# Performance work log

Hardware: AMD Instinct MI355X
Metric: run time of the kernel (lower is better)

## Reference

```python
import jax, jax.numpy as jnp
import numpy as np

B = 64
D_IN = 4000            # reduced from hardcoded 40000 to fit memory budget (see notes)
N_NODES = 200
ADJ = N_NODES * N_NODES  # 40000 entries per adjacency
E_PER = ADJ // 4         # strictly > 0.75-quantile of 40000 continuous values == top 10000
NEG_SLOPE = 0.2          # GATv2Conv default leaky_relu slope
LN_EPS = 1e-5


def _gelu(x):
    return jax.nn.gelu(x, approximate=False)  # torch F.gelu default = exact erf


def _gatv2(x, src, dst, valid, Wl, bl, Wr, br, att, bias, heads, ch, concat, n):
    # PyG GATv2Conv (share_weights=False): xl = lin_l(x), xr = lin_r(x)
    xl = (x @ Wl + bl).reshape(n, heads, ch)
    xr = (x @ Wr + br).reshape(n, heads, ch)
    e = jax.nn.leaky_relu(xl[src] + xr[dst], NEG_SLOPE)        # [E,H,C]
    logits = jnp.einsum('ehc,hc->eh', e, att)                   # [E,H]
    if valid is not None:
        logits = jnp.where(valid[:, None], logits, -jnp.inf)
    m = jax.ops.segment_max(logits, dst, num_segments=n)
    m = jnp.where(jnp.isfinite(m), m, 0.0)
    ex = jnp.exp(logits - m[dst])
    if valid is not None:
        ex = jnp.where(valid[:, None], ex, 0.0)
    denom = jax.ops.segment_sum(ex, dst, num_segments=n)
    alpha = ex / (denom[dst] + 1e-16)                            # scatter-softmax per target
    out = jax.ops.segment_sum(xl[src] * alpha[..., None], dst, num_segments=n)
    out = out.reshape(n, heads * ch) if concat else out.mean(axis=1)
    return out + bias


def _forward(raw_fc, gbW, gbb, feW1, feb1, feW2, feb2, ln_g, ln_b,
             W1l, b1l, W1r, b1r, att1, bias1,
             W2l, b2l, W2r, b2r, att2, bias2,
             W3l, b3l, W3r, b3r, att3, bias3):
    b = raw_fc.shape[0]
    n = b * N_NODES
    # ---- build_graph ----
    adj = jax.nn.sigmoid(raw_fc @ gbW + gbb).reshape(b, N_NODES, N_NODES)
    adj = (adj + jnp.swapaxes(adj, 1, 2)) * 0.5
    means = adj.mean(axis=2)                    # [B,200]
    stds = jnp.std(adj, axis=2, ddof=1) + 1e-6  # torch std is unbiased
    base = jnp.stack([means, stds], axis=-1).reshape(n, 2)
    h = _gelu(base @ feW1 + feb1) @ feW2 + feb2
    mu = h.mean(-1, keepdims=True)
    var = h.var(-1, keepdims=True)
    x = (h - mu) / jnp.sqrt(var + LN_EPS) * ln_g + ln_b          # LayerNorm(16)
    _, idx = jax.lax.top_k(adj.reshape(b, ADJ), E_PER)           # [B, 10000]
    row = idx // N_NODES
    col = idx % N_NODES
    offs = (jnp.arange(b) * N_NODES)[:, None]
    src = (row + offs).reshape(-1)
    dst = (col + offs).reshape(-1)
    # ---- GAT stack (eval mode: dropout = identity) ----
    x = _gelu(_gatv2(x, src, dst, None, W1l, b1l, W1r, b1r, att1, bias1, 8, 128, True, n))
    # layers 2/3 have add_self_loops=True: remove existing self loops, append one per node
    loops = jnp.arange(n)
    src2 = jnp.concatenate([src, loops])
    dst2 = jnp.concatenate([dst, loops])
    valid2 = jnp.concatenate([src != dst, jnp.ones((n,), bool)])
    x = _gelu(_gatv2(x, src2, dst2, valid2, W2l, b2l, W2r, b2r, att2, bias2, 4, 256, True, n))
    x = _gelu(_gatv2(x, src2, dst2, valid2, W3l, b3l, W3r, b3r, att3, bias3, 1, 512, False, n))
    # global_mean_pool: exactly 200 nodes per graph, contiguous ordering
    return x.reshape(b, N_NODES, 512).mean(axis=1)


def setup_inputs() -> dict:
    key = jax.random.key(0)
    ks = jax.random.split(key, 16)
    f32 = jnp.float32
    def gl(k, shape, fan_in):
        return jax.random.normal(k, shape, f32) / np.sqrt(fan_in)
    inp = {}
    inp['raw_fc'] = jax.random.normal(ks[0], (B, D_IN), f32)
    inp['gbW'] = gl(ks[1], (D_IN, ADJ), D_IN)
    inp['gbb'] = jnp.zeros((ADJ,), f32)
    inp['feW1'] = gl(ks[2], (2, 8), 2);      inp['feb1'] = jnp.zeros((8,), f32)
    inp['feW2'] = gl(ks[3], (8, 16), 8);     inp['feb2'] = jnp.zeros((16,), f32)
    inp['ln_g'] = jnp.ones((16,), f32);      inp['ln_b'] = jnp.zeros((16,), f32)
    inp['W1l'] = gl(ks[4], (16, 8 * 128), 16);   inp['b1l'] = jnp.zeros((8 * 128,), f32)
    inp['W1r'] = gl(ks[5], (16, 8 * 128), 16);   inp['b1r'] = jnp.zeros((8 * 128,), f32)
    inp['att1'] = gl(ks[6], (8, 128), 128);      inp['bias1'] = jnp.zeros((8 * 128,), f32)
    inp['W2l'] = gl(ks[7], (1024, 4 * 256), 1024); inp['b2l'] = jnp.zeros((4 * 256,), f32)
    inp['W2r'] = gl(ks[8], (1024, 4 * 256), 1024); inp['b2r'] = jnp.zeros((4 * 256,), f32)
    inp['att2'] = gl(ks[9], (4, 256), 256);        inp['bias2'] = jnp.zeros((4 * 256,), f32)
    inp['W3l'] = gl(ks[10], (1024, 512), 1024);    inp['b3l'] = jnp.zeros((512,), f32)
    inp['W3r'] = gl(ks[11], (1024, 512), 1024);    inp['b3r'] = jnp.zeros((512,), f32)
    inp['att3'] = gl(ks[12], (1, 512), 512);       inp['bias3'] = jnp.zeros((512,), f32)
    return inp


def reference(raw_fc, gbW, gbb, feW1, feb1, feW2, feb2, ln_g, ln_b,
              W1l, b1l, W1r, b1r, att1, bias1,
              W2l, b2l, W2r, b2r, att2, bias2,
              W3l, b3l, W3r, b3r, att3, bias3):
    return _forward(raw_fc, gbW, gbb, feW1, feb1, feW2, feb2, ln_g, ln_b,
                    W1l, b1l, W1r, b1r, att1, bias1,
                    W2l, b2l, W2r, b2r, att2, bias2,
                    W3l, b3l, W3r, b3r, att3, bias3)
```

## Files before the change

### kernel.cpp

```cpp
#include <hip/hip_runtime.h>
#include <hip/hip_fp16.h>
#include <math.h>
#include <cstdint>
#include <cstddef>

#define NGRAPH 64
#define NN 200
#define ADJN 40000
#define DIN 4000
#define NNODE 12800

typedef float    f32x4 __attribute__((ext_vector_type(4)));
typedef _Float16 f16x8 __attribute__((ext_vector_type(8)));
typedef _Float16 f16x4 __attribute__((ext_vector_type(4)));
typedef _Float16 f16x2 __attribute__((ext_vector_type(2)));
typedef short    bf8v  __attribute__((ext_vector_type(8)));
typedef short    bf4v  __attribute__((ext_vector_type(4)));

union BF8U  { bf8v v; bf4v h[2]; };
union F16X8U{ f16x8 v; f16x4 h[2]; f16x2 p[4]; };
union U4F   { uint4 u; unsigned w[4]; };

__device__ __forceinline__ unsigned short f2bf(float f) {
  unsigned u = __float_as_uint(f);
  return (unsigned short)((u + 0x7fffu + ((u >> 16) & 1u)) >> 16);
}
__device__ __forceinline__ float bf2f(unsigned short s) {
  return __uint_as_float(((unsigned)s) << 16);
}
__device__ __forceinline__ float gelu_f(float x) {
  return x * 0.5f * (1.0f + erff(x * 0.70710678118654752f));
}

#if defined(__has_builtin)
#if __has_builtin(__builtin_amdgcn_fdot2)
#define FDOT2(a, b, c) __builtin_amdgcn_fdot2((a), (b), (c), false)
#endif
#endif
#ifndef FDOT2
#define FDOT2(a, b, c) ((c) + (float)(a)[0] * (float)(b)[0] + (float)(a)[1] * (float)(b)[1])
#endif

__device__ __forceinline__ void glds16(const _Float16* g, _Float16* l) {
  __builtin_amdgcn_global_load_lds(
      (const __attribute__((address_space(1))) void*)g,
      (__attribute__((address_space(3))) void*)l, 16, 0, 0);
}

__global__ __launch_bounds__(256) void prep_A(const float* __restrict__ A,
                                              short* __restrict__ Ahi,
                                              short* __restrict__ Alo) {
  const int i = blockIdx.x * 256 + threadIdx.x;
  const float v = A[i];
  const unsigned short h = f2bf(v);
  Ahi[i] = (short)h;
  Alo[i] = (short)f2bf(v - bf2f(h));
}

__global__ __launch_bounds__(256) void transp_all(
    const float* __restrict__ W2l, const float* __restrict__ W2r,
    const float* __restrict__ W3l, const float* __restrict__ W3r,
    _Float16* __restrict__ T2l, _Float16* __restrict__ T2r,
    _Float16* __restrict__ T3l, _Float16* __restrict__ T3r) {
  __shared__ float tile[32][33];
  const int z = blockIdx.z;
  if (z >= 2 && blockIdx.y >= 16) return;
  const float* src = (z == 0) ? W2l : (z == 1) ? W2r : (z == 2) ? W3l : W3r;
  _Float16* dst = (z == 0) ? T2l : (z == 1) ? T2r : (z == 2) ? T3l : T3r;
  const int N = (z < 2) ? 1024 : 512;
  const int K = 1024;
  const int bk = blockIdx.x * 32, bn = blockIdx.y * 32;
  const int tx = threadIdx.x & 31, ty = threadIdx.x >> 5;
#pragma unroll
  for (int r = 0; r < 32; r += 8) tile[ty + r][tx] = src[(size_t)(bk + ty + r) * N + bn + tx];
  __syncthreads();
#pragma unroll
  for (int r = 0; r < 32; r += 8)
    dst[(size_t)(bn + ty + r) * K + bk + tx] = (_Float16)tile[tx][ty + r];
}

#define BA_LOADW(WV, K0)                                                        \
  _Pragma("unroll") for (int q = 0; q < 8; ++q)                                 \
    WV[q] = W[(size_t)((K0) + kgrp * 8 + q) * ADJN + n0 + nn];

#define BA_CONV(PB, WV)                                                         \
  { bf4v h0, h1, l0, l1;                                                        \
    _Pragma("unroll") for (int i = 0; i < 4; ++i) {                             \
      unsigned short hh = (unsigned short)(__float_as_uint(WV[i]) >> 16);       \
      h0[i] = (short)hh;                                                        \
      l0[i] = (short)f2bf(WV[i] - bf2f(hh));                                    \
    }                                                                           \
    _Pragma("unroll") for (int i = 0; i < 4; ++i) {                             \
      unsigned short hh = (unsigned short)(__float_as_uint(WV[4 + i]) >> 16);   \
      h1[i] = (short)hh;                                                        \
      l1[i] = (short)f2bf(WV[4 + i] - bf2f(hh));                                \
    }                                                                           \
    *(bf4v*)(Wh[PB] + nn * 44 + kgrp * 8)     = h0;                             \
    *(bf4v*)(Wh[PB] + nn * 44 + kgrp * 8 + 4) = h1;                             \
    *(bf4v*)(Wl[PB] + nn * 44 + kgrp * 8)     = l0;                             \
    *(bf4v*)(Wl[PB] + nn * 44 + kgrp * 8 + 4) = l1;                             \
  }

#define BA_MFMA(PB, AHC, ALC)                                                   \
  _Pragma("unroll") for (int j = 0; j < 4; ++j) {                               \
    const int bc = (j * 16 + (lane & 15)) * 44 + kb;                            \
    BF8U bh, bl;                                                                \
    bh.h[0] = *(const bf4v*)(Wh[PB] + bc);                                      \
    bh.h[1] = *(const bf4v*)(Wh[PB] + bc + 4);                                  \
    bl.h[0] = *(const bf4v*)(Wl[PB] + bc);                                      \
    bl.h[1] = *(const bf4v*)(Wl[PB] + bc + 4);                                  \
    acc[j] = __builtin_amdgcn_mfma_f32_16x16x32_bf16(AHC, bh.v, acc[j], 0, 0, 0); \
    acc[j] = __builtin_amdgcn_mfma_f32_16x16x32_bf16(AHC, bl.v, acc[j], 0, 0, 0); \
    acc[j] = __builtin_amdgcn_mfma_f32_16x16x32_bf16(ALC, bh.v, acc[j], 0, 0, 0); \
  }

#define BA_LOADA(AH, AL, K0)                                                    \
  AH = *(const bf8v*)(Ahi + (size_t)arow * DIN + (K0) + kb);                    \
  AL = *(const bf8v*)(Alo + (size_t)arow * DIN + (K0) + kb);

__global__ __launch_bounds__(256) void build_adj(
    const short* __restrict__ Ahi, const short* __restrict__ Alo,
    const float* __restrict__ W, const float* __restrict__ bias,
    float* __restrict__ adj) {
  __shared__ short Wh[2][64 * 44], Wl[2][64 * 44];
  const int t = threadIdx.x, wave = t >> 6, lane = t & 63;
  const int n0 = blockIdx.x * 64;
  const int nn = t & 63, kgrp = t >> 6;
  const int kb = (lane >> 4) * 8;
  const int arow = wave * 16 + (lane & 15);
  f32x4 acc[4] = {};
  float wva[8], wvb[8];
  bf8v ahs0, als0, ahs1, als1;
  BA_LOADW(wva, 0)
  BA_LOADA(ahs0, als0, 0)
  BA_LOADW(wvb, 32)
  BA_LOADA(ahs1, als1, 32)
  BA_CONV(0, wva)
  for (int it = 0; it < 124; it += 2) {
    __syncthreads();
    {
      const bf8v ahc = ahs0, alc = als0;
      if (it + 2 < 125) {
        const int k2 = (it + 2) * 32;
        BA_LOADW(wva, k2)
        BA_LOADA(ahs0, als0, k2)
      }
      BA_MFMA(0, ahc, alc)
      BA_CONV(1, wvb)
    }
    __syncthreads();
    {
      const bf8v ahc = ahs1, alc = als1;
      if (it + 3 < 125) {
        const int k2 = (it + 3) * 32;
        BA_LOADW(wvb, k2)
        BA_LOADA(ahs1, als1, k2)
      }
      BA_MFMA(1, ahc, alc)
      if (it + 2 < 125) BA_CONV(0, wva)
    }
  }
  __syncthreads();
  BA_MFMA(0, ahs0, als0)
#pragma unroll
  for (int j = 0; j < 4; ++j) {
    const int col = n0 + j * 16 + (lane & 15);
    const float bb = bias[col];
#pragma unroll
    for (int vv = 0; vv < 4; ++vv) {
      const int row = wave * 16 + (lane >> 4) * 4 + vv;
      float x = acc[j][vv] + bb;
      adj[(size_t)row * ADJN + col] = 1.0f / (1.0f + __expf(-x));
    }
  }
}

__global__ __launch_bounds__(256) void symmetrize(const float* __restrict__ adj,
                                                  float* __restrict__ adjS) {
  __shared__ float tl[64][65];
  const int g = blockIdx.x;
  const int i0 = (blockIdx.y >> 2) * 64, j0 = (blockIdx.y & 3) * 64;
  const int tx = threadIdx.x & 63, ty = threadIdx.x >> 6;
  const float* ag = adj + (size_t)g * ADJN;
#pragma unroll
  for (int r = 0; r < 64; r += 4) {
    const int jr = j0 + ty + r;
    tl[ty + r][tx] = (jr < NN && i0 + tx < NN) ? ag[jr * NN + i0 + tx] : 0.f;
  }
  __syncthreads();
#pragma unroll
  for (int r = 0; r < 64; r += 4) {
    const int i = i0 + ty + r, j = j0 + tx;
    if (i < NN && j < NN)
      adjS[(size_t)g * ADJN + i * NN + j] = 0.5f * (ag[i * NN + j] + tl[tx][ty + r]);
  }
}

__global__ __launch_bounds__(256) void rowstats(const float* __restrict__ adjS,
                                                float* __restrict__ meanv,
                                                float* __restrict__ stdv) {
  const int row = blockIdx.x * 4 + (threadIdx.x >> 6);
  const int lane = threadIdx.x & 63;
  const float* r = adjS + (size_t)row * NN;
  float s = 0.f, q = 0.f;
#pragma unroll
  for (int k = 0; k < 4; ++k) {
    int i = k * 64 + lane;
    if (i < NN) { float v = r[i]; s += v; q += v * v; }
  }
#pragma unroll
  for (int off = 32; off > 0; off >>= 1) { s += __shfl_xor(s, off); q += __shfl_xor(q, off); }
  if (lane == 0) {
    float m = s * (1.0f / 200.0f);
    float var = (q - 200.0f * m * m) * (1.0f / 199.0f);
    var = fmaxf(var, 0.f);
    meanv[row] = m;
    stdv[row] = sqrtf(var) + 1e-6f;
  }
}

__global__ __launch_bounds__(1024) void radix_lists(
    const float* __restrict__ adjS,
    int* __restrict__ cnt1, int* __restrict__ cnt2,
    unsigned char* __restrict__ list1, unsigned char* __restrict__ list2) {
  __shared__ unsigned hist[4 * 2048];
  __shared__ unsigned s_pref, s_cA;
  const int g = blockIdx.x, t = threadIdx.x, lane = t & 63, wave = t >> 6;
  const float* v = adjS + (size_t)g * ADJN;
  unsigned prefix = 0, pmask = 0, cA = 0;
  const int shifts[3] = {20, 9, 0};
  const int widths[3] = {2048, 2048, 512};
  for (int pass = 0; pass < 3; ++pass) {
    const int nb = widths[pass], sh = shifts[pass];
    for (int i = t; i < 8192; i += 1024) hist[i] = 0u;
    __syncthreads();
    const int cpy = (lane & 3) * 2048;
    for (int e = t; e < ADJN; e += 1024) {
      unsigned u = __float_as_uint(v[e]);
      if ((u & pmask) == prefix) atomicAdd(&hist[cpy + ((u >> sh) & (nb - 1))], 1u);
    }
    __syncthreads();
    if (t < 64) {
      const int CH = nb >> 6;
      unsigned lsum = 0;
      for (int i = 0; i < CH; ++i) {
        const int b = t * CH + i;
        lsum += hist[b] + hist[2048 + b] + hist[4096 + b] + hist[6144 + b];
      }
      unsigned s = lsum;
#pragma unroll
      for (int off = 1; off < 64; off <<= 1) {
        unsigned o = __shfl_down(s, off);
        if (lane + off < 64) s += o;
      }
      const unsigned need = 10000u - cA;
      unsigned sn = __shfl_down(s, 1);
      const unsigned snext = (lane == 63) ? 0u : sn;
      if (s >= need && snext < need) {
        unsigned cum = snext;
        int bsel = t * CH;
        for (int i = CH - 1; i >= 0; --i) {
          const int b = t * CH + i;
          unsigned hb = hist[b] + hist[2048 + b] + hist[4096 + b] + hist[6144 + b];
          if (cum + hb >= need) { bsel = b; break; }
          cum += hb;
        }
        s_pref = prefix | ((unsigned)bsel << sh);
        s_cA = cA + cum;
      }
    }
    __syncthreads();
    prefix = s_pref; cA = s_cA;
    pmask |= (unsigned)(widths[pass] - 1) << sh;
    __syncthreads();
  }
  const float tv = __uint_as_float(prefix);
  for (int j = wave; j < NN; j += 16) {
    const float* row = adjS + (size_t)g * ADJN + (size_t)j * NN;
    unsigned char* l1 = list1 + ((size_t)g * NN + j) * NN;
    unsigned char* l2 = list2 + ((size_t)g * NN + j) * NN;
    int c1 = 0, c2 = 0;
#pragma unroll
    for (int r = 0; r < 4; ++r) {
      int i = r * 64 + lane;
      bool p1 = false, p2 = false;
      if (i < NN) { float vv = row[i]; p1 = (vv >= tv); p2 = p1 && (i != j); }
      unsigned long long b1 = __ballot(p1);
      unsigned long long b2 = __ballot(p2);
      unsigned long long below = (lane == 0) ? 0ull : ((~0ull) >> (64 - lane));
      if (p1) l1[c1 + __popcll(b1 & below)] = (unsigned char)i;
      if (p2) l2[c2 + __popcll(b2 & below)] = (unsigned char)i;
      c1 += (int)__popcll(b1); c2 += (int)__popcll(b2);
    }
    if (lane == 0) {
      l2[c2] = (unsigned char)j;
      cnt1[g * NN + j] = c1;
      cnt2[g * NN + j] = c2 + 1;
    }
  }
}

__global__ __launch_bounds__(256) void lin16_fused(
    const float* __restrict__ meanv, const float* __restrict__ stdv,
    const float* __restrict__ feW1, const float* __restrict__ feb1,
    const float* __restrict__ feW2, const float* __restrict__ feb2,
    const float* __restrict__ ln_g, const float* __restrict__ ln_b,
    const float* __restrict__ Wl, const float* __restrict__ bl,
    const float* __restrict__ Wr, const float* __restrict__ br,
    _Float16* __restrict__ outl, _Float16* __restrict__ outr) {
  __shared__ _Float16 Wt[1024 * 20];
  __shared__ float x0s[16][17];
  const int t = threadIdx.x, wave = t >> 6, lane = t & 63;
  const int mbase = blockIdx.x * 16;
  {
    const int n = t >> 4, o = t & 15;
    const float mu = meanv[mbase + n], sd = stdv[mbase + n];
    float h1[8];
#pragma unroll
    for (int k = 0; k < 8; ++k) h1[k] = gelu_f(mu * feW1[k] + sd * feW1[8 + k] + feb1[k]);
    float h2 = feb2[o];
#pragma unroll
    for (int k = 0; k < 8; ++k) h2 += h1[k] * feW2[k * 16 + o];
    float s = h2;
#pragma unroll
    for (int off = 1; off < 16; off <<= 1) s += __shfl_xor(s, off);
    s *= (1.0f / 16.0f);
    const float d = h2 - s;
    float vv = d * d;
#pragma unroll
    for (int off = 1; off < 16; off <<= 1) vv += __shfl_xor(vv, off);
    vv *= (1.0f / 16.0f);
    x0s[n][o] = d * (1.0f / sqrtf(vv + 1e-5f)) * ln_g[o] + ln_b[o];
  }
  __syncthreads();
  const int mrow = lane & 15, kg = lane >> 4;
  F16X8U af;
#pragma unroll
  for (int q = 0; q < 8; ++q) af.v[q] = (_Float16)0.f;
  if (kg < 2) {
#pragma unroll
    for (int q = 0; q < 8; ++q) af.v[q] = (_Float16)x0s[mrow][kg * 8 + q];
  }
#pragma unroll
  for (int mat = 0; mat < 2; ++mat) {
    if (mat) __syncthreads();
    const float* Wsrc = mat ? Wr : Wl;
    for (int i = t; i < 4096; i += 256) {
      const int k = i >> 8, n4 = (i & 255) * 4;
      float4 wv = *(const float4*)(Wsrc + (size_t)k * 1024 + n4);
      Wt[(n4 + 0) * 20 + k] = (_Float16)wv.x;
      Wt[(n4 + 1) * 20 + k] = (_Float16)wv.y;
      Wt[(n4 + 2) * 20 + k] = (_Float16)wv.z;
      Wt[(n4 + 3) * 20 + k] = (_Float16)wv.w;
    }
    __syncthreads();
    const float* bias = mat ? br : bl;
    _Float16* out = mat ? outr : outl;
#pragma unroll
    for (int nt = 0; nt < 16; ++nt) {
      const int n0 = wave * 256 + nt * 16;
      F16X8U bfv;
#pragma unroll
      for (int q = 0; q < 8; ++q) bfv.v[q] = (_Float16)0.f;
      if (kg < 2) bfv.v = *(const f16x8*)(Wt + (n0 + mrow) * 20 + kg * 8);
      f32x4 acc = {};
      acc = __builtin_amdgcn_mfma_f32_16x16x32_f16(af.v, bfv.v, acc, 0, 0, 0);
      const int col = n0 + mrow;
      const float bb = bias[col];
#pragma unroll
      for (int j = 0; j < 4; ++j)
        out[(size_t)(mbase + kg * 4 + j) * 1024 + col] = (_Float16)(acc[j] + bb);
    }
  }
}

__global__ __launch_bounds__(256, 2) void gemm_nt(
    const _Float16* __restrict__ A,
    const _Float16* __restrict__ Bt0, const _Float16* __restrict__ Bt1,
    const float* __restrict__ b0, const float* __restrict__ b1,
    _Float16* __restrict__ out0, _Float16* __restrict__ out1,
    int Nhalf, int tilesPerHalf) {
  __shared__ _Float16 As[2][128 * 64];
  __shared__ _Float16 Bs[2][128 * 64];
  const int mbase = blockIdx.y * 128;
  const int hsel = blockIdx.x / tilesPerHalf;
  const int ncol0 = (blockIdx.x % tilesPerHalf) * 128;
  const _Float16* Bt = hsel ? Bt1 : Bt0;
  const float* bias = hsel ? b1 : b0;
  _Float16* out = hsel ? out1 : out0;
  const int t = threadIdx.x, wave = t >> 6, lane = t & 63;
  const int wm = wave >> 1, wn = wave & 1;
  f32x4 acc[4][4] = {};
  const int srow = lane >> 3;
  const int sg = (lane & 7) ^ srow;
#pragma unroll
  for (int c = 0; c < 4; ++c) {
    const int rbase = wave * 32 + c * 8;
    glds16(A + (size_t)(mbase + rbase + srow) * 1024 + sg * 8, As[0] + rbase * 64);
    glds16(Bt + (size_t)(ncol0 + rbase + srow) * 1024 + sg * 8, Bs[0] + rbase * 64);
  }
  __syncthreads();
  for (int kt = 0; kt < 16; ++kt) {
    const int p = kt & 1;
    if (kt < 15) {
      const int k0 = (kt + 1) * 64;
#pragma unroll
      for (int c = 0; c < 4; ++c) {
        const int rbase = wave * 32 + c * 8;
        glds16(A + (size_t)(mbase + rbase + srow) * 1024 + k0 + sg * 8, As[p ^ 1] + rbase * 64);
        glds16(Bt + (size_t)(ncol0 + rbase + srow) * 1024 + k0 + sg * 8, Bs[p ^ 1] + rbase * 64);
      }
    }
#pragma unroll
    for (int ks = 0; ks < 2; ++ks) {
      F16X8U af[4], bfv[4];
#pragma unroll
      for (int m = 0; m < 4; ++m) {
        const int row = wm * 64 + m * 16 + (lane & 15);
        const int kk = ks * 32 + (lane >> 4) * 8;
        af[m].v = *(const f16x8*)(As[p] + row * 64 + (kk ^ ((row & 7) << 3)));
      }
#pragma unroll
      for (int j = 0; j < 4; ++j) {
        const int row = wn * 64 + j * 16 + (lane & 15);
        const int kk = ks * 32 + (lane >> 4) * 8;
        bfv[j].v = *(const f16x8*)(Bs[p] + row * 64 + (kk ^ ((row & 7) << 3)));
      }
#pragma unroll
      for (int j = 0; j < 4; ++j)
#pragma unroll
        for (int m = 0; m < 4; ++m)
          acc[m][j] = __builtin_amdgcn_mfma_f32_16x16x32_f16(af[m].v, bfv[j].v, acc[m][j], 0, 0, 0);
    }
    __syncthreads();
  }
#pragma unroll
  for (int j = 0; j < 4; ++j) {
    const int col = ncol0 + wn * 64 + j * 16 + (lane & 15);
    const float bb = bias[col];
#pragma unroll
    for (int m = 0; m < 4; ++m) {
#pragma unroll
      for (int vv = 0; vv < 4; ++vv) {
        const int row = mbase + wm * 64 + m * 16 + (lane >> 4) * 4 + vv;
        out[(size_t)row * Nhalf + col] = (_Float16)(acc[m][j][vv] + bb);
      }
    }
  }
}

template <int C, int HC>
__global__ __launch_bounds__(1024, 4) void gat_layer(
    const _Float16* __restrict__ xlb, const _Float16* __restrict__ xrb,
    const float* __restrict__ attw, const float* __restrict__ biasw,
    const int* __restrict__ cnts, const unsigned char* __restrict__ lists,
    _Float16* __restrict__ outb) {
  extern __shared__ char smem[];
  constexpr int XLB = 200 * C * 2;
  constexpr int XRW = 16 * C * 2;
  _Float16* xr_s = (_Float16*)(smem + XLB);
  unsigned* awp = (unsigned*)(smem + XLB + XRW);
  unsigned* att_s = (unsigned*)(smem + XLB + XRW + 12800);
  const int g = blockIdx.x;
  const int hd = blockIdx.y;
  const int t = threadIdx.x, wave = t >> 6, lane = t & 63;
  constexpr int NGR = C / 8;
  constexpr int GRP = (C == 128) ? 16 : 32;
  constexpr int NG = 64 / GRP;
  const int grp = lane / GRP, li = lane % GRP;
  const int rc = lane & (NGR - 1) & 31;

  for (int ch = t; ch < 200 * NGR; ch += 1024) {
    const int node = ch / NGR, cc = (ch % NGR) * 8;
    *(f16x8*)(smem + (node * C + cc) * 2) =
        *(const f16x8*)(xlb + (size_t)(g * 200 + node) * HC + hd * C + cc);
  }
  for (int i = t; i < C / 2; i += 1024) {
    f16x2 a;
    a[0] = (_Float16)attw[hd * C + 2 * i];
    a[1] = (_Float16)attw[hd * C + 2 * i + 1];
    att_s[i] = __builtin_bit_cast(unsigned, a);
  }
  __syncthreads();

  _Float16* xr_w = xr_s + wave * C;
  const uint4* att4 = (const uint4*)att_s;
  f16x8 xrreg;
  if (lane < NGR)
    xrreg = *(const f16x8*)(xrb + (size_t)(g * 200 + wave) * HC + hd * C + lane * 8);

  for (int jj = wave; jj < 200; jj += 16) {
    const int gn = g * 200 + jj;
    const int cnt = cnts[gn];
    const unsigned char* lst = lists + (size_t)gn * NN;
    if (lane < NGR) {
      *(f16x8*)(xr_w + lane * 8) = xrreg;
      if (jj + 16 < 200)
        xrreg = *(const f16x8*)(xrb + (size_t)(gn + 16) * HC + hd * C + lane * 8);
    }
    float lg[4] = {-INFINITY, -INFINITY, -INFINITY, -INFINITY};
    int sreg[4];
#pragma unroll
    for (int r = 0; r < 4; ++r) {
      const int e = (r << 6) + lane;
      if (e < cnt) {
        const int s = lst[e];
        sreg[r] = s;
        const _Float16* xrow = (const _Float16*)(smem) + s * C;
        float accv[4] = {0.f, 0.f, 0.f, 0.f};
#pragma unroll 4
        for (int gi0 = 0; gi0 < NGR; ++gi0) {
          const int gi = (gi0 + rc) & (NGR - 1);
          const int cc = gi * 8;
          F16X8U xa, raa;
          xa.v = *(const f16x8*)(xrow + cc);
          raa.v = *(const f16x8*)(xr_w + cc);
          U4F av; av.u = att4[gi];
#pragma unroll
          for (int pq = 0; pq < 4; ++pq) {
            f16x2 z = xa.p[pq] + raa.p[pq];
            f16x2 zs = z * (_Float16)0.2f;
            f16x2 m = __builtin_elementwise_max(z, zs);
            accv[pq] = FDOT2(__builtin_bit_cast(f16x2, av.w[pq]), m, accv[pq]);
          }
        }
        lg[r] = (accv[0] + accv[1]) + (accv[2] + accv[3]);
      }
    }
    float mloc = fmaxf(fmaxf(lg[0], lg[1]), fmaxf(lg[2], lg[3]));
#pragma unroll
    for (int off = 32; off > 0; off >>= 1) mloc = fmaxf(mloc, __shfl_xor(mloc, off));
    float ex[4]; float ps = 0.f;
#pragma unroll
    for (int r = 0; r < 4; ++r) { ex[r] = __expf(lg[r] - mloc); ps += ex[r]; }
#pragma unroll
    for (int off = 32; off > 0; off >>= 1) ps += __shfl_xor(ps, off);
    const float denom = ps + 1e-16f;
#pragma unroll
    for (int r = 0; r < 4; ++r) {
      const int e = (r << 6) + lane;
      if (e < cnt) {
        const unsigned short ab =
            __builtin_bit_cast(unsigned short, (_Float16)(ex[r] / denom));
        awp[wave * 200 + e] = ((unsigned)ab << 16) | (unsigned)sreg[r];
      }
    }
    float o[8] = {};
    for (int e0 = 0; e0 < cnt; e0 += NG) {
      const int e = e0 + grp;
      if (e < cnt) {
        const unsigned v = awp[wave * 200 + e];
        const int s = v & 0xFF;
        const float a =
            (float)__builtin_bit_cast(_Float16, (unsigned short)(v >> 16));
        f16x8 xv = *(const f16x8*)((const _Float16*)smem + s * C + li * 8);
#pragma unroll
        for (int q = 0; q < 8; ++q) o[q] += a * (float)xv[q];
      }
    }
#pragma unroll
    for (int q = 0; q < 8; ++q) {
      if constexpr (GRP == 16) o[q] += __shfl_xor(o[q], 16);
      o[q] += __shfl_xor(o[q], 32);
    }
    if (grp == 0) {
      const int colb = hd * C + li * 8;
      f16x8 ov;
#pragma unroll
      for (int q = 0; q < 8; ++q) ov[q] = (_Float16)gelu_f(o[q] + biasw[colb + q]);
      *(f16x8*)(outb + (size_t)gn * HC + colb) = ov;
    }
  }
}

__global__ __launch_bounds__(1024, 4) void gat_l3(
    const _Float16* __restrict__ xlb, const _Float16* __restrict__ xrb,
    const float* __restrict__ attw, const float* __restrict__ biasw,
    const int* __restrict__ cnts, const unsigned char* __restrict__ lists,
    float* __restrict__ psum) {
  extern __shared__ char smem[];
  _Float16* xr_s = (_Float16*)(smem + 51200);
  float* plog = (float*)(smem + 64000);
  unsigned* plogp = (unsigned*)(smem + 64000);
  unsigned* att_s = (unsigned*)(smem + 104000);
  const int g = blockIdx.x, range = blockIdx.y, r0 = range * 50;
  const int t = threadIdx.x, wave = t >> 6, lane = t & 63;
  const int grp = lane >> 4, li = lane & 15;
  const int rc = lane & 15;
  const uint4* att4 = (const uint4*)att_s;

  for (int chunk = 0; chunk < 4; ++chunk) {
    if (chunk) __syncthreads();
    for (int ch = t; ch < 200 * 16; ch += 1024) {
      const int node = ch >> 4, cc = (ch & 15) * 8;
      *(f16x8*)(smem + (node * 128 + cc) * 2) =
          *(const f16x8*)(xlb + (size_t)(g * 200 + node) * 512 + chunk * 128 + cc);
    }
    for (int ch = t; ch < 50 * 16; ch += 1024) {
      const int node = ch >> 4, cc = (ch & 15) * 8;
      *(f16x8*)(xr_s + node * 128 + cc) =
          *(const f16x8*)(xrb + (size_t)(g * 200 + r0 + node) * 512 + chunk * 128 + cc);
    }
    for (int i = t; i < 64; i += 1024) {
      f16x2 a;
      a[0] = (_Float16)attw[chunk * 128 + 2 * i];
      a[1] = (_Float16)attw[chunk * 128 + 2 * i + 1];
      att_s[i] = __builtin_bit_cast(unsigned, a);
    }
    __syncthreads();
    for (int jj = wave; jj < 50; jj += 16) {
      const int gn = g * 200 + r0 + jj;
      const int cnt = cnts[gn];
      const unsigned char* lst = lists + (size_t)gn * NN;
#pragma unroll
      for (int r = 0; r < 4; ++r) {
        const int e = (r << 6) + lane;
        if (e < cnt) {
          const int s = lst[e];
          const _Float16* xrow = (const _Float16*)(smem) + s * 128;
          float accv[4] = {0.f, 0.f, 0.f, 0.f};
#pragma unroll 4
          for (int gi0 = 0; gi0 < 16; ++gi0) {
            const int gi = (gi0 + rc) & 15;
            const int cc = gi * 8;
            F16X8U xa, raa;
            xa.v = *(const f16x8*)(xrow + cc);
            raa.v = *(const f16x8*)(xr_s + jj * 128 + cc);
            U4F av; av.u = att4[gi];
#pragma unroll
            for (int pq = 0; pq < 4; ++pq) {
              f16x2 z = xa.p[pq] + raa.p[pq];
              f16x2 zs = z * (_Float16)0.2f;
              f16x2 m = __builtin_elementwise_max(z, zs);
              accv[pq] = FDOT2(__builtin_bit_cast(f16x2, av.w[pq]), m, accv[pq]);
            }
          }
          const float acc = (accv[0] + accv[1]) + (accv[2] + accv[3]);
          if (chunk == 0) plog[jj * 200 + e] = acc;
          else plog[jj * 200 + e] += acc;
        }
      }
    }
  }
  __syncthreads();
  for (int jj = wave; jj < 50; jj += 16) {
    const int gn = g * 200 + r0 + jj;
    const int cnt = cnts[gn];
    const unsigned char* lst = lists + (size_t)gn * NN;
    float lg[4] = {-INFINITY, -INFINITY, -INFINITY, -INFINITY};
#pragma unroll
    for (int r = 0; r < 4; ++r) {
      const int e = (r << 6) + lane;
      if (e < cnt) lg[r] = plog[jj * 200 + e];
    }
    float mloc = fmaxf(fmaxf(lg[0], lg[1]), fmaxf(lg[2], lg[3]));
#pragma unroll
    for (int off = 32; off > 0; off >>= 1) mloc = fmaxf(mloc, __shfl_xor(mloc, off));
    float ex[4]; float ps = 0.f;
#pragma unroll
    for (int r = 0; r < 4; ++r) { ex[r] = __expf(lg[r] - mloc); ps += ex[r]; }
#pragma unroll
    for (int off = 32; off > 0; off >>= 1) ps += __shfl_xor(ps, off);
    const float denom = ps + 1e-16f;
#pragma unroll
    for (int r = 0; r < 4; ++r) {
      const int e = (r << 6) + lane;
      if (e < cnt) {
        const unsigned short ab =
            __builtin_bit_cast(unsigned short, (_Float16)(ex[r] / denom));
        plogp[jj * 200 + e] = ((unsigned)ab << 16) | (unsigned)lst[e];
      }
    }
  }
  for (int chunk = 0; chunk < 4; ++chunk) {
    __syncthreads();
    for (int ch = t; ch < 200 * 16; ch += 1024) {
      const int node = ch >> 4, cc = (ch & 15) * 8;
      *(f16x8*)(smem + (node * 128 + cc) * 2) =
          *(const f16x8*)(xlb + (size_t)(g * 200 + node) * 512 + chunk * 128 + cc);
    }
    __syncthreads();
    float p[8] = {};
    for (int jj = wave; jj < 50; jj += 16) {
      const int gn = g * 200 + r0 + jj;
      const int cnt = cnts[gn];
      float o[8] = {};
      for (int e0 = 0; e0 < cnt; e0 += 4) {
        const int e = e0 + grp;
        if (e < cnt) {
          const unsigned v = plogp[jj * 200 + e];
          const int s = v & 0xFF;
          const float a =
              (float)__builtin_bit_cast(_Float16, (unsigned short)(v >> 16));
          f16x8 xv = *(const f16x8*)((const _Float16*)smem + s * 128 + li * 8);
#pragma unroll
          for (int q = 0; q < 8; ++q) o[q] += a * (float)xv[q];
        }
      }
#pragma unroll
      for (int q = 0; q < 8; ++q) {
        o[q] += __shfl_xor(o[q], 16);
        o[q] += __shfl_xor(o[q], 32);
      }
      if (grp == 0) {
        const int colb = chunk * 128 + li * 8;
#pragma unroll
        for (int q = 0; q < 8; ++q) p[q] += gelu_f(o[q] + biasw[colb + q]);
      }
    }
    if (grp == 0) {
      const int slot = range * 16 + wave;
      float* pd = psum + ((size_t)slot * 64 + g) * 512 + chunk * 128 + li * 8;
      float4 a0 = {p[0], p[1], p[2], p[3]};
      float4 a1 = {p[4], p[5], p[6], p[7]};
      *(float4*)pd = a0;
      *(float4*)(pd + 4) = a1;
    }
  }
}

__global__ void finalize(const float* __restrict__ psum, float* __restrict__ out) {
  const int idx = blockIdx.x * 256 + threadIdx.x;
  float s = 0.f;
#pragma unroll
  for (int k = 0; k < 64; ++k) s += psum[(size_t)k * 32768 + idx];
  out[idx] = s * 0.005f;
}

extern "C" void kernel_launch(void* const* d_in, const int* in_sizes, int n_in,
                              void* d_out, int out_size, void* d_ws, size_t ws_size,
                              hipStream_t stream) {
  const float* raw_fc = (const float*)d_in[0];
  const float* gbW = (const float*)d_in[1];
  const float* gbb = (const float*)d_in[2];
  const float* feW1 = (const float*)d_in[3];
  const float* feb1 = (const float*)d_in[4];
  const float* feW2 = (const float*)d_in[5];
  const float* feb2 = (const float*)d_in[6];
  const float* ln_g = (const float*)d_in[7];
  const float* ln_b = (const float*)d_in[8];
  const float* W1l = (const float*)d_in[9];  const float* b1l = (const float*)d_in[10];
  const float* W1r = (const float*)d_in[11]; const float* b1r = (const float*)d_in[12];
  const float* att1 = (const float*)d_in[13]; const float* bias1 = (const float*)d_in[14];
  const float* W2l = (const float*)d_in[15]; const float* b2l = (const float*)d_in[16];
  const float* W2r = (const float*)d_in[17]; const float* b2r = (const float*)d_in[18];
  const float* att2 = (const float*)d_in[19]; const float* bias2 = (const float*)d_in[20];
  const float* W3l = (const float*)d_in[21]; const float* b3l = (const float*)d_in[22];
  const float* W3r = (const float*)d_in[23]; const float* b3r = (const float*)d_in[24];
  const float* att3 = (const float*)d_in[25]; const float* bias3 = (const float*)d_in[26];

  if (ws_size < 121000000) return;

  char* w = (char*)d_ws;
  float* adj   = (float*)(w + 0);
  float* adjS  = (float*)(w + 10240000);
  float* meanv = (float*)(w + 20480000);
  float* stdv  = (float*)(w + 20531200);
  int* cnt1    = (int*)(w + 21401856);
  int* cnt2    = (int*)(w + 21453056);
  unsigned char* list1 = (unsigned char*)(w + 21504256);
  unsigned char* list2 = (unsigned char*)(w + 24064256);
  _Float16* bufA = (_Float16*)(w + 26624256);
  _Float16* bufB = (_Float16*)(w + 52838656);
  _Float16* bufC = (_Float16*)(w + 79053056);
  float* psum = (float*)(w + 105267456);
  short* Ahi  = (short*)(w + 113656064);
  short* Alo  = (short*)(w + 114168064);
  _Float16* Wt2l = (_Float16*)(w + 114680064);
  _Float16* Wt2r = (_Float16*)(w + 116777216);
  _Float16* Wt3l = (_Float16*)(w + 118874368);
  _Float16* Wt3r = (_Float16*)(w + 119922944);

  const int SMEM_L1 = 68352;
  const int SMEM_L2 = 123904;
  const int SMEM_L3 = 104256;
  hipFuncSetAttribute((const void*)gat_layer<128, 1024>,
                      hipFuncAttributeMaxDynamicSharedMemorySize, SMEM_L1);
  hipFuncSetAttribute((const void*)gat_layer<256, 1024>,
                      hipFuncAttributeMaxDynamicSharedMemorySize, SMEM_L2);
  hipFuncSetAttribute((const void*)gat_l3,
                      hipFuncAttributeMaxDynamicSharedMemorySize, SMEM_L3);

  prep_A<<<1000, 256, 0, stream>>>(raw_fc, Ahi, Alo);
  transp_all<<<dim3(32, 32, 4), 256, 0, stream>>>(W2l, W2r, W3l, W3r, Wt2l, Wt2r, Wt3l, Wt3r);
  build_adj<<<625, 256, 0, stream>>>(Ahi, Alo, gbW, gbb, adj);
  symmetrize<<<dim3(64, 16), 256, 0, stream>>>(adj, adjS);
  rowstats<<<3200, 256, 0, stream>>>(adjS, meanv, stdv);
  radix_lists<<<64, 1024, 0, stream>>>(adjS, cnt1, cnt2, list1, list2);
  lin16_fused<<<800, 256, 0, stream>>>(meanv, stdv, feW1, feb1, feW2, feb2, ln_g, ln_b,
                                       W1l, b1l, W1r, b1r, bufA, bufB);
  gat_layer<128, 1024><<<dim3(64, 8), 1024, SMEM_L1, stream>>>(
      bufA, bufB, att1, bias1, cnt1, list1, bufC);
  gemm_nt<<<dim3(16, 100), 256, 0, stream>>>(bufC, Wt2l, Wt2r, b2l, b2r, bufA, bufB, 1024, 8);
  gat_layer<256, 1024><<<dim3(64, 4), 1024, SMEM_L2, stream>>>(
      bufA, bufB, att2, bias2, cnt2, list2, bufC);
  gemm_nt<<<dim3(8, 100), 256, 0, stream>>>(bufC, Wt3l, Wt3r, b3l, b3r, bufA, bufB, 512, 4);
  gat_l3<<<dim3(64, 4), 1024, SMEM_L3, stream>>>(bufA, bufB, att3, bias3, cnt2, list2, psum);
  finalize<<<128, 256, 0, stream>>>(psum, (float*)d_out);
}
```

Before: 906.8 us.

## Process two target nodes per wave in GAT logit loops for ILP

Each wave in the GAT layer kernels now handles two target nodes per iteration (j and j+16) and computes their attention logits in one interleaved loop, so LDS reads and dot products for the two nodes can overlap. The xr row slots per wave double, and LDS sizes for layers 1 and 2 grow to match. The old register prefetch of the next xr row is replaced by direct loads at the start of each iteration. Unroll pragmas are added to the aggregation loops. The cost is higher register pressure, divergent doA/doB predicates and more LDS per block, which may reduce occupancy.

```diff
diff --git a/kernel.cpp b/kernel.cpp
--- a/kernel.cpp
+++ b/kernel.cpp
@@ -457,7 +457,7 @@
     _Float16* __restrict__ outb) {
   extern __shared__ char smem[];
   constexpr int XLB = 200 * C * 2;
-  constexpr int XRW = 16 * C * 2;
+  constexpr int XRW = 32 * C * 2;
   _Float16* xr_s = (_Float16*)(smem + XLB);
   unsigned* awp = (unsigned*)(smem + XLB + XRW);
   unsigned* att_s = (unsigned*)(smem + XLB + XRW + 12800);
@@ -483,92 +483,168 @@
   }
   __syncthreads();
 
-  _Float16* xr_w = xr_s + wave * C;
+  _Float16* xrA = xr_s + wave * 2 * C;
+  _Float16* xrB = xrA + C;
   const uint4* att4 = (const uint4*)att_s;
-  f16x8 xrreg;
-  if (lane < NGR)
-    xrreg = *(const f16x8*)(xrb + (size_t)(g * 200 + wave) * HC + hd * C + lane * 8);
-
-  for (int jj = wave; jj < 200; jj += 16) {
-    const int gn = g * 200 + jj;
-    const int cnt = cnts[gn];
-    const unsigned char* lst = lists + (size_t)gn * NN;
-    if (lane < NGR) {
-      *(f16x8*)(xr_w + lane * 8) = xrreg;
-      if (jj + 16 < 200)
-        xrreg = *(const f16x8*)(xrb + (size_t)(gn + 16) * HC + hd * C + lane * 8);
-    }
-    float lg[4] = {-INFINITY, -INFINITY, -INFINITY, -INFINITY};
-    int sreg[4];
+
+  for (int jj = wave; jj < 200; jj += 32) {
+    const int jB = jj + 16;
+    const bool hasB = (jB < 200);
+    const int gnA = g * 200 + jj;
+    const int gnB = g * 200 + jB;
+    const int cntA = cnts[gnA];
+    const int cntB = hasB ? cnts[gnB] : 0;
+    const unsigned char* lstA = lists + (size_t)gnA * NN;
+    const unsigned char* lstB = lists + (size_t)gnB * NN;
+    {
+      const int which = lane / NGR;
+      const int gr = lane % NGR;
+      if (which == 0 || (which == 1 && hasB)) {
+        const int node = which ? gnB : gnA;
+        f16x8 v = *(const f16x8*)(xrb + (size_t)node * HC + hd * C + gr * 8);
+        *(f16x8*)(xrA + which * C + gr * 8) = v;
+      }
+    }
+    float lgA[4] = {-INFINITY, -INFINITY, -INFINITY, -INFINITY};
+    float lgB[4] = {-INFINITY, -INFINITY, -INFINITY, -INFINITY};
+    int srA[4], srB[4];
 #pragma unroll
     for (int r = 0; r < 4; ++r) {
       const int e = (r << 6) + lane;
-      if (e < cnt) {
-        const int s = lst[e];
-        sreg[r] = s;
-        const _Float16* xrow = (const _Float16*)(smem) + s * C;
-        float accv[4] = {0.f, 0.f, 0.f, 0.f};
+      const bool doA = e < cntA, doB = e < cntB;
+      if (doA | doB) {
+        int sA = 0, sB = 0;
+        if (doA) { sA = lstA[e]; srA[r] = sA; }
+        if (doB) { sB = lstB[e]; srB[r] = sB; }
+        const _Float16* xrowA = (const _Float16*)(smem) + sA * C;
+        const _Float16* xrowB = (const _Float16*)(smem) + sB * C;
+        float aA[4] = {0.f, 0.f, 0.f, 0.f};
+        float aB[4] = {0.f, 0.f, 0.f, 0.f};
 #pragma unroll 4
         for (int gi0 = 0; gi0 < NGR; ++gi0) {
           const int gi = (gi0 + rc) & (NGR - 1);
           const int cc = gi * 8;
-          F16X8U xa, raa;
-          xa.v = *(const f16x8*)(xrow + cc);
-          raa.v = *(const f16x8*)(xr_w + cc);
           U4F av; av.u = att4[gi];
-#pragma unroll
-          for (int pq = 0; pq < 4; ++pq) {
-            f16x2 z = xa.p[pq] + raa.p[pq];
-            f16x2 zs = z * (_Float16)0.2f;
-            f16x2 m = __builtin_elementwise_max(z, zs);
-            accv[pq] = FDOT2(__builtin_bit_cast(f16x2, av.w[pq]), m, accv[pq]);
+          if (doA) {
+            F16X8U xa, raa;
+            xa.v = *(const f16x8*)(xrowA + cc);
+            raa.v = *(const f16x8*)(xrA + cc);
+#pragma unroll
+            for (int pq = 0; pq < 4; ++pq) {
+              f16x2 z = xa.p[pq] + raa.p[pq];
+              f16x2 zs = z * (_Float16)0.2f;
+              f16x2 m = __builtin_elementwise_max(z, zs);
+              aA[pq] = FDOT2(__builtin_bit_cast(f16x2, av.w[pq]), m, aA[pq]);
+            }
+          }
+          if (doB) {
+            F16X8U xb, rbb;
+            xb.v = *(const f16x8*)(xrowB + cc);
+            rbb.v = *(const f16x8*)(xrB + cc);
+#pragma unroll
+            for (int pq = 0; pq < 4; ++pq) {
+              f16x2 z = xb.p[pq] + rbb.p[pq];
+              f16x2 zs = z * (_Float16)0.2f;
+              f16x2 m = __builtin_elementwise_max(z, zs);
+              aB[pq] = FDOT2(__builtin_bit_cast(f16x2, av.w[pq]), m, aB[pq]);
+            }
           }
         }
-        lg[r] = (accv[0] + accv[1]) + (accv[2] + accv[3]);
-      }
-    }
-    float mloc = fmaxf(fmaxf(lg[0], lg[1]), fmaxf(lg[2], lg[3]));
-#pragma unroll
-    for (int off = 32; off > 0; off >>= 1) mloc = fmaxf(mloc, __shfl_xor(mloc, off));
-    float ex[4]; float ps = 0.f;
-#pragma unroll
-    for (int r = 0; r < 4; ++r) { ex[r] = __expf(lg[r] - mloc); ps += ex[r]; }
-#pragma unroll
-    for (int off = 32; off > 0; off >>= 1) ps += __shfl_xor(ps, off);
-    const float denom = ps + 1e-16f;
-#pragma unroll
-    for (int r = 0; r < 4; ++r) {
-      const int e = (r << 6) + lane;
-      if (e < cnt) {
-        const unsigned short ab =
-            __builtin_bit_cast(unsigned short, (_Float16)(ex[r] / denom));
-        awp[wave * 200 + e] = ((unsigned)ab << 16) | (unsigned)sreg[r];
-      }
-    }
-    float o[8] = {};
-    for (int e0 = 0; e0 < cnt; e0 += NG) {
-      const int e = e0 + grp;
-      if (e < cnt) {
-        const unsigned v = awp[wave * 200 + e];
-        const int s = v & 0xFF;
-        const float a =
-            (float)__builtin_bit_cast(_Float16, (unsigned short)(v >> 16));
-        f16x8 xv = *(const f16x8*)((const _Float16*)smem + s * C + li * 8);
-#pragma unroll
-        for (int q = 0; q < 8; ++q) o[q] += a * (float)xv[q];
-      }
-    }
-#pragma unroll
-    for (int q = 0; q < 8; ++q) {
-      if constexpr (GRP == 16) o[q] += __shfl_xor(o[q], 16);
-      o[q] += __shfl_xor(o[q], 32);
-    }
-    if (grp == 0) {
-      const int colb = hd * C + li * 8;
-      f16x8 ov;
-#pragma unroll
-      for (int q = 0; q < 8; ++q) ov[q] = (_Float16)gelu_f(o[q] + biasw[colb + q]);
-      *(f16x8*)(outb + (size_t)gn * HC + colb) = ov;
+        if (doA) lgA[r] = (aA[0] + aA[1]) + (aA[2] + aA[3]);
+        if (doB) lgB[r] = (aB[0] + aB[1]) + (aB[2] + aB[3]);
+      }
+    }
+    {
+      float mloc = fmaxf(fmaxf(lgA[0], lgA[1]), fmaxf(lgA[2], lgA[3]));
+#pragma unroll
+      for (int off = 32; off > 0; off >>= 1) mloc = fmaxf(mloc, __shfl_xor(mloc, off));
+      float ex[4]; float ps = 0.f;
+#pragma unroll
+      for (int r = 0; r < 4; ++r) { ex[r] = __expf(lgA[r] - mloc); ps += ex[r]; }
+#pragma unroll
+      for (int off = 32; off > 0; off >>= 1) ps += __shfl_xor(ps, off);
+      const float denom = ps + 1e-16f;
+#pragma unroll
+      for (int r = 0; r < 4; ++r) {
+        const int e = (r << 6) + lane;
+        if (e < cntA) {
+          const unsigned short ab =
+              __builtin_bit_cast(unsigned short, (_Float16)(ex[r] / denom));
+          awp[wave * 200 + e] = ((unsigned)ab << 16) | (unsigned)srA[r];
+        }
+      }
+      float o[8] = {};
+#pragma unroll 4
+      for (int e0 = 0; e0 < cntA; e0 += NG) {
+        const int e = e0 + grp;
+        if (e < cntA) {
+          const unsigned v = awp[wave * 200 + e];
+          const int s = v & 0xFF;
+          const float a =
+              (float)__builtin_bit_cast(_Float16, (unsigned short)(v >> 16));
+          f16x8 xv = *(const f16x8*)((const _Float16*)smem + s * C + li * 8);
+#pragma unroll
+          for (int q = 0; q < 8; ++q) o[q] += a * (float)xv[q];
+        }
+      }
+#pragma unroll
+      for (int q = 0; q < 8; ++q) {
+        if constexpr (GRP == 16) o[q] += __shfl_xor(o[q], 16);
+        o[q] += __shfl_xor(o[q], 32);
+      }
+      if (grp == 0) {
+        const int colb = hd * C + li * 8;
+        f16x8 ov;
+#pragma unroll
+        for (int q = 0; q < 8; ++q) ov[q] = (_Float16)gelu_f(o[q] + biasw[colb + q]);
+        *(f16x8*)(outb + (size_t)gnA * HC + colb) = ov;
+      }
+    }
+    if (hasB) {
+      float mloc = fmaxf(fmaxf(lgB[0], lgB[1]), fmaxf(lgB[2], lgB[3]));
+#pragma unroll
+      for (int off = 32; off > 0; off >>= 1) mloc = fmaxf(mloc, __shfl_xor(mloc, off));
+      float ex[4]; float ps = 0.f;
+#pragma unroll
+      for (int r = 0; r < 4; ++r) { ex[r] = __expf(lgB[r] - mloc); ps += ex[r]; }
+#pragma unroll
+      for (int off = 32; off > 0; off >>= 1) ps += __shfl_xor(ps, off);
+      const float denom = ps + 1e-16f;
+#pragma unroll
+      for (int r = 0; r < 4; ++r) {
+        const int e = (r << 6) + lane;
+        if (e < cntB) {
+          const unsigned short ab =
+              __builtin_bit_cast(unsigned short, (_Float16)(ex[r] / denom));
+          awp[wave * 200 + e] = ((unsigned)ab << 16) | (unsigned)srB[r];
+        }
+      }
+      float o[8] = {};
+#pragma unroll 4
+      for (int e0 = 0; e0 < cntB; e0 += NG) {
+        const int e = e0 + grp;
+        if (e < cntB) {
+          const unsigned v = awp[wave * 200 + e];
+          const int s = v & 0xFF;
+          const float a =
+              (float)__builtin_bit_cast(_Float16, (unsigned short)(v >> 16));
+          f16x8 xv = *(const f16x8*)((const _Float16*)smem + s * C + li * 8);
+#pragma unroll
+          for (int q = 0; q < 8; ++q) o[q] += a * (float)xv[q];
+        }
+      }
+#pragma unroll
+      for (int q = 0; q < 8; ++q) {
+        if constexpr (GRP == 16) o[q] += __shfl_xor(o[q], 16);
+        o[q] += __shfl_xor(o[q], 32);
+      }
+      if (grp == 0) {
+        const int colb = hd * C + li * 8;
+        f16x8 ov;
+#pragma unroll
+        for (int q = 0; q < 8; ++q) ov[q] = (_Float16)gelu_f(o[q] + biasw[colb + q]);
+        *(f16x8*)(outb + (size_t)gnB * HC + colb) = ov;
+      }
     }
   }
 }
@@ -608,36 +684,67 @@
       att_s[i] = __builtin_bit_cast(unsigned, a);
     }
     __syncthreads();
-    for (int jj = wave; jj < 50; jj += 16) {
-      const int gn = g * 200 + r0 + jj;
-      const int cnt = cnts[gn];
-      const unsigned char* lst = lists + (size_t)gn * NN;
+    for (int jj = wave; jj < 50; jj += 32) {
+      const int jB = jj + 16;
+      const bool hasB = (jB < 50);
+      const int gnA = g * 200 + r0 + jj;
+      const int gnB = g * 200 + r0 + jB;
+      const int cntA = cnts[gnA];
+      const int cntB = hasB ? cnts[gnB] : 0;
+      const unsigned char* lstA = lists + (size_t)gnA * NN;
+      const unsigned char* lstB = lists + (size_t)gnB * NN;
 #pragma unroll
       for (int r = 0; r < 4; ++r) {
         const int e = (r << 6) + lane;
-        if (e < cnt) {
-          const int s = lst[e];
-          const _Float16* xrow = (const _Float16*)(smem) + s * 128;
-          float accv[4] = {0.f, 0.f, 0.f, 0.f};
+        const bool doA = e < cntA, doB = e < cntB;
+        if (doA | doB) {
+          int sA = 0, sB = 0;
+          if (doA) sA = lstA[e];
+          if (doB) sB = lstB[e];
+          const _Float16* xrowA = (const _Float16*)(smem) + sA * 128;
+          const _Float16* xrowB = (const _Float16*)(smem) + sB * 128;
+          float aA[4] = {0.f, 0.f, 0.f, 0.f};
+          float aB[4] = {0.f, 0.f, 0.f, 0.f};
 #pragma unroll 4
           for (int gi0 = 0; gi0 < 16; ++gi0) {
             const int gi = (gi0 + rc) & 15;
             const int cc = gi * 8;
-            F16X8U xa, raa;
-            xa.v = *(const f16x8*)(xrow + cc);
-            raa.v = *(const f16x8*)(xr_s + jj * 128 + cc);
             U4F av; av.u = att4[gi];
-#pragma unroll
-            for (int pq = 0; pq < 4; ++pq) {
-              f16x2 z = xa.p[pq] + raa.p[pq];
-              f16x2 zs = z * (_Float16)0.2f;
-              f16x2 m = __builtin_elementwise_max(z, zs);
-              accv[pq] = FDOT2(__builtin_bit_cast(f16x2, av.w[pq]), m, accv[pq]);
+            if (doA) {
+              F16X8U xa, raa;
+              xa.v = *(const f16x8*)(xrowA + cc);
+              raa.v = *(const f16x8*)(xr_s + jj * 128 + cc);
+#pragma unroll
+              for (int pq = 0; pq < 4; ++pq) {
+                f16x2 z = xa.p[pq] + raa.p[pq];
+                f16x2 zs = z * (_Float16)0.2f;
+                f16x2 m = __builtin_elementwise_max(z, zs);
+                aA[pq] = FDOT2(__builtin_bit_cast(f16x2, av.w[pq]), m, aA[pq]);
+              }
+            }
+            if (doB) {
+              F16X8U xb, rbb;
+              xb.v = *(const f16x8*)(xrowB + cc);
+              rbb.v = *(const f16x8*)(xr_s + jB * 128 + cc);
+#pragma unroll
+              for (int pq = 0; pq < 4; ++pq) {
+                f16x2 z = xb.p[pq] + rbb.p[pq];
+                f16x2 zs = z * (_Float16)0.2f;
+                f16x2 m = __builtin_elementwise_max(z, zs);
+                aB[pq] = FDOT2(__builtin_bit_cast(f16x2, av.w[pq]), m, aB[pq]);
+              }
             }
           }
-          const float acc = (accv[0] + accv[1]) + (accv[2] + accv[3]);
-          if (chunk == 0) plog[jj * 200 + e] = acc;
-          else plog[jj * 200 + e] += acc;
+          if (doA) {
+            const float acc = (aA[0] + aA[1]) + (aA[2] + aA[3]);
+            if (chunk == 0) plog[jj * 200 + e] = acc;
+            else plog[jj * 200 + e] += acc;
+          }
+          if (doB) {
+            const float acc = (aB[0] + aB[1]) + (aB[2] + aB[3]);
+            if (chunk == 0) plog[jB * 200 + e] = acc;
+            else plog[jB * 200 + e] += acc;
+          }
         }
       }
     }
@@ -685,6 +792,7 @@
       const int gn = g * 200 + r0 + jj;
       const int cnt = cnts[gn];
       float o[8] = {};
+#pragma unroll 4
       for (int e0 = 0; e0 < cnt; e0 += 4) {
         const int e = e0 + grp;
         if (e < cnt) {
@@ -771,8 +879,8 @@
   _Float16* Wt3l = (_Float16*)(w + 118874368);
   _Float16* Wt3r = (_Float16*)(w + 119922944);
 
-  const int SMEM_L1 = 68352;
-  const int SMEM_L2 = 123904;
+  const int SMEM_L1 = 72448;
+  const int SMEM_L2 = 132096;
   const int SMEM_L3 = 104256;
   hipFuncSetAttribute((const void*)gat_layer<128, 1024>,
                       hipFuncAttributeMaxDynamicSharedMemorySize, SMEM_L1);
```

Result: slower. 941.6 us (+3.8%).
